# Kernel optimization log

Hardware: AMD Instinct MI355X
Metric: run time of the kernel (lower is better)

The kernel has to match this reference:

```python
import jax, jax.numpy as jnp
import numpy as np

# Module hyperparams (match init_kwargs)
NUM_EXPERTS = 64
DIM = 1024
RANK = 16
ALPHA = 1.0
SCALE = ALPHA / RANK


def setup_inputs() -> dict:
    key = jax.random.key(0)
    k1, k2, k3, k4 = jax.random.split(key, 4)
    B, K, M, D, R = 8, 8, 512, DIM, RANK
    z = jax.random.normal(k1, (B, K, M, D), dtype=jnp.float32)
    A_all = jax.random.normal(k2, (NUM_EXPERTS, D, R), dtype=jnp.float32) * 0.02
    B_all = jax.random.normal(k3, (NUM_EXPERTS, R, D), dtype=jnp.float32) * 0.02
    expert_indices = jax.random.randint(k4, (K,), 0, NUM_EXPERTS, dtype=jnp.int64) if jax.config.jax_enable_x64 else jax.random.randint(k4, (K,), 0, NUM_EXPERTS, dtype=jnp.int32)
    return {"z": z, "A_all": A_all, "B_all": B_all, "expert_indices": expert_indices}


def reference(z, A_all, B_all, expert_indices):
    # Gather per-expert LoRA factors: A [K, D, R], B [K, R, D]
    A = A_all[expert_indices]
    Bm = B_all[expert_indices]
    # Low-rank down/up projection per (batch, expert)
    down = jnp.einsum('bkmd,kdr->bkmr', z, A)   # [B, K, M, R]
    up = jnp.einsum('bkmr,krd->bkmd', down, Bm)  # [B, K, M, D]
    return up * SCALE
```

## Files before the change

kernel.cpp:

```cpp
#include <hip/hip_runtime.h>
#include <hip/hip_bf16.h>

#define DD 1024
#define RR 16
#define MM 512
#define KK 8
#define BB 8
#define SCALE_F 0.0625f

#define TT 2
#define BT 8
#define TILES 8

template <int LEN, int XOR>
__device__ __forceinline__ void fold(float (&v)[32], int lane) {
    const bool hi = (lane & XOR) != 0;
#pragma unroll
    for (int i = 0; i < LEN / 2; ++i) {
        const float keep = hi ? v[2 * i + 1] : v[2 * i];
        const float send = hi ? v[2 * i] : v[2 * i + 1];
        v[i] = keep + __shfl_xor(send, XOR, 64);
    }
}

__global__ __launch_bounds__(256, 2)
void lora_down(const float* __restrict__ z, const float* __restrict__ A_all,
               const int* __restrict__ eidx, float* __restrict__ down)
{
    __shared__ float At[RR][DD];

    const int mc = blockIdx.x;
    const int b  = blockIdx.y;
    const int k  = blockIdx.z;
    const int e  = eidx[k];

    const float* __restrict__ Ae = A_all + (size_t)e * (DD * RR);

    for (int f4 = threadIdx.x; f4 < DD * RR / 4; f4 += 256) {
        const int f = f4 << 2;
        const float4 v = *reinterpret_cast<const float4*>(Ae + f);
        const int d = f >> 4, r = f & 15;
        At[r + 0][d] = v.x;
        At[r + 1][d] = v.y;
        At[r + 2][d] = v.z;
        At[r + 3][d] = v.w;
    }
    __syncthreads();

    const int wave = threadIdx.x >> 6;
    const int lane = threadIdx.x & 63;
    const size_t rowbk = ((size_t)b * KK + k) * MM;
    const int mbase = mc * 64 + wave * TT;
    const float* __restrict__ zlane = z + (rowbk + mbase) * DD + lane * 4;

    float4 bufA[TT][4], bufB[TT][4];

    auto load_tile = [&](float4 (&buf)[TT][4], int it) {
#pragma unroll
        for (int t = 0; t < TT; ++t) {
            const float* p = zlane + (size_t)(it * BT + t) * DD;
#pragma unroll
            for (int s = 0; s < 4; ++s)
                buf[t][s] = *reinterpret_cast<const float4*>(p + s * 256);
        }
    };

    auto compute_store = [&](const float4 (&buf)[TT][4], int it) {
        float v[32];
#pragma unroll
        for (int i = 0; i < 32; ++i) v[i] = 0.f;
#pragma unroll
        for (int s = 0; s < 4; ++s) {
            const int dbase = s * 256 + lane * 4;
#pragma unroll
            for (int r = 0; r < RR; ++r) {
                const float4 a = *reinterpret_cast<const float4*>(&At[r][dbase]);
#pragma unroll
                for (int t = 0; t < TT; ++t) {
                    const float4 zv = buf[t][s];
                    float acc = v[t * 16 + r];
                    acc = fmaf(zv.x, a.x, acc);
                    acc = fmaf(zv.y, a.y, acc);
                    acc = fmaf(zv.z, a.z, acc);
                    acc = fmaf(zv.w, a.w, acc);
                    v[t * 16 + r] = acc;
                }
            }
        }
        fold<32, 1>(v, lane);
        fold<16, 2>(v, lane);
        fold<8, 4>(v, lane);
        fold<4, 8>(v, lane);
        fold<2, 16>(v, lane);
        const float total = v[0] + __shfl_xor(v[0], 32, 64);
        if (lane < 32)
            down[(rowbk + mbase + it * BT) * RR + lane] = total;
    };

    load_tile(bufA, 0);
#pragma unroll 1
    for (int ip = 0; ip < TILES / 2; ++ip) {
        load_tile(bufB, 2 * ip + 1);
        compute_store(bufA, 2 * ip);
        if (ip < TILES / 2 - 1) load_tile(bufA, 2 * ip + 2);
        compute_store(bufB, 2 * ip + 1);
    }
}

__global__ __launch_bounds__(256, 2)
void lora_up(const float* __restrict__ down, const float* __restrict__ B_all,
             const int* __restrict__ eidx, float* __restrict__ out)
{
    __shared__ float Bl[RR][DD];

    const int mc = blockIdx.x;
    const int b  = blockIdx.y;
    const int k  = blockIdx.z;
    const int e  = eidx[k];

    const float* __restrict__ Be = B_all + (size_t)e * (RR * DD);
    for (int f4 = threadIdx.x; f4 < RR * DD / 4; f4 += 256)
        *reinterpret_cast<float4*>(&Bl[0][0] + (f4 << 2)) =
            *reinterpret_cast<const float4*>(Be + (f4 << 2));
    __syncthreads();

    const int wave = threadIdx.x >> 6;
    const int lane = threadIdx.x & 63;
    const size_t rowbk = ((size_t)b * KK + k) * MM;
    const int mbase = mc * 64 + wave * TT;

    float cA[32], cB[32];

    auto load_c = [&](float (&c)[32], int it) {
        const float4* dp = reinterpret_cast<const float4*>(down + (rowbk + mbase + it * BT) * RR);
#pragma unroll
        for (int i = 0; i < 8; ++i) {
            const float4 v = dp[i];
            c[i * 4 + 0] = v.x;
            c[i * 4 + 1] = v.y;
            c[i * 4 + 2] = v.z;
            c[i * 4 + 3] = v.w;
        }
    };

    auto compute_store = [&](const float (&c)[32], int it) {
#pragma unroll
        for (int s = 0; s < 4; ++s) {
            const int dbase = s * 256 + lane * 4;
            float4 o[TT];
#pragma unroll
            for (int t = 0; t < TT; ++t) o[t] = make_float4(0.f, 0.f, 0.f, 0.f);
#pragma unroll
            for (int r = 0; r < RR; ++r) {
                const float4 bv = *reinterpret_cast<const float4*>(&Bl[r][dbase]);
#pragma unroll
                for (int t = 0; t < TT; ++t) {
                    const float cf = c[t * 16 + r];
                    o[t].x = fmaf(cf, bv.x, o[t].x);
                    o[t].y = fmaf(cf, bv.y, o[t].y);
                    o[t].z = fmaf(cf, bv.z, o[t].z);
                    o[t].w = fmaf(cf, bv.w, o[t].w);
                }
            }
#pragma unroll
            for (int t = 0; t < TT; ++t) {
                float4 res;
                res.x = o[t].x * SCALE_F;
                res.y = o[t].y * SCALE_F;
                res.z = o[t].z * SCALE_F;
                res.w = o[t].w * SCALE_F;
                *reinterpret_cast<float4*>(out + (rowbk + mbase + it * BT + t) * DD + dbase) = res;
            }
        }
    };

    load_c(cA, 0);
#pragma unroll 1
    for (int ip = 0; ip < TILES / 2; ++ip) {
        load_c(cB, 2 * ip + 1);
        compute_store(cA, 2 * ip);
        if (ip < TILES / 2 - 1) load_c(cA, 2 * ip + 2);
        compute_store(cB, 2 * ip + 1);
    }
}

extern "C" void kernel_launch(void* const* d_in, const int* in_sizes, int n_in,
                              void* d_out, int out_size, void* d_ws, size_t ws_size,
                              hipStream_t stream) {
    const float* z     = (const float*)d_in[0];
    const float* A_all = (const float*)d_in[1];
    const float* B_all = (const float*)d_in[2];
    const int*   eidx  = (const int*)d_in[3];
    float* out  = (float*)d_out;
    float* down = (float*)d_ws;

    dim3 grid(MM / 64, BB, KK);
    dim3 block(256);

    lora_down<<<grid, block, 0, stream>>>(z, A_all, eidx, down);
    lora_up<<<grid, block, 0, stream>>>(down, B_all, eidx, out);
}
```

Before: 512.0 us.

## Fuse LoRA down and up projections into one kernel with half-D shared tiles

Merges the down and up projection kernels into one. The down result stays in shared memory instead of going through a global workspace. Each block now handles 32 rows and loads the expert A and B factors in two half-width shared tiles, so shared memory use drops and more blocks can fit per CU (launch bounds raised to 4). The trade-off is that A and B are reloaded more often per row, and extra barriers are added between the phases.

```diff
diff --git a/kernel.cpp b/kernel.cpp
--- a/kernel.cpp
+++ b/kernel.cpp
@@ -2,15 +2,14 @@
 #include <hip/hip_bf16.h>
 
 #define DD 1024
+#define HD 512
 #define RR 16
 #define MM 512
 #define KK 8
 #define BB 8
+#define RB 32
 #define SCALE_F 0.0625f
-
-#define TT 2
-#define BT 8
-#define TILES 8
+#define LDP (HD + 4)
 
 template <int LEN, int XOR>
 __device__ __forceinline__ void fold(float (&v)[32], int lane) {
@@ -23,164 +22,133 @@
     }
 }
 
-__global__ __launch_bounds__(256, 2)
-void lora_down(const float* __restrict__ z, const float* __restrict__ A_all,
-               const int* __restrict__ eidx, float* __restrict__ down)
+__global__ __launch_bounds__(256, 4)
+void lora_fused(const float* __restrict__ z, const float* __restrict__ A_all,
+                const float* __restrict__ B_all, const int* __restrict__ eidx,
+                float* __restrict__ out)
 {
-    __shared__ float At[RR][DD];
+    __shared__ float Sh[RR][LDP];
+    __shared__ float dn[RB][RR];
 
-    const int mc = blockIdx.x;
-    const int b  = blockIdx.y;
-    const int k  = blockIdx.z;
-    const int e  = eidx[k];
+    const int mc = blockIdx.x, b = blockIdx.y, k = blockIdx.z;
+    const int e = eidx[k];
+    const int tid  = threadIdx.x;
+    const int wave = tid >> 6, lane = tid & 63;
+
+    const size_t rowbase = ((size_t)b * KK + k) * MM + (size_t)mc * RB;
+    const int wrow = wave * 8;
 
     const float* __restrict__ Ae = A_all + (size_t)e * (DD * RR);
+    const float* __restrict__ Be = B_all + (size_t)e * (RR * DD);
 
-    for (int f4 = threadIdx.x; f4 < DD * RR / 4; f4 += 256) {
-        const int f = f4 << 2;
-        const float4 v = *reinterpret_cast<const float4*>(Ae + f);
-        const int d = f >> 4, r = f & 15;
-        At[r + 0][d] = v.x;
-        At[r + 1][d] = v.y;
-        At[r + 2][d] = v.z;
-        At[r + 3][d] = v.w;
-    }
-    __syncthreads();
+#pragma unroll 1
+    for (int h = 0; h < 2; ++h) {
+        for (int idx = tid; idx < HD * RR / 4; idx += 256) {
+            const int f = h * (HD * RR) + idx * 4;
+            const float4 v4 = *reinterpret_cast<const float4*>(Ae + f);
+            const int d = (f >> 4) - h * HD;
+            const int r = f & 15;
+            Sh[r + 0][d] = v4.x; Sh[r + 1][d] = v4.y;
+            Sh[r + 2][d] = v4.z; Sh[r + 3][d] = v4.w;
+        }
+        __syncthreads();
 
-    const int wave = threadIdx.x >> 6;
-    const int lane = threadIdx.x & 63;
-    const size_t rowbk = ((size_t)b * KK + k) * MM;
-    const int mbase = mc * 64 + wave * TT;
-    const float* __restrict__ zlane = z + (rowbk + mbase) * DD + lane * 4;
+        const float* zl = z + (rowbase + wrow) * DD + h * HD + lane * 4;
+        float4 bufA[2][2], bufB[2][2];
 
-    float4 bufA[TT][4], bufB[TT][4];
-
-    auto load_tile = [&](float4 (&buf)[TT][4], int it) {
+        auto ldt = [&](float4 (&bf)[2][2], int t0) {
 #pragma unroll
-        for (int t = 0; t < TT; ++t) {
-            const float* p = zlane + (size_t)(it * BT + t) * DD;
+            for (int t = 0; t < 2; ++t)
 #pragma unroll
-            for (int s = 0; s < 4; ++s)
-                buf[t][s] = *reinterpret_cast<const float4*>(p + s * 256);
-        }
-    };
-
-    auto compute_store = [&](const float4 (&buf)[TT][4], int it) {
-        float v[32];
+                for (int s = 0; s < 2; ++s)
+                    bf[t][s] = *reinterpret_cast<const float4*>(
+                        zl + (size_t)(t0 + t) * DD + s * 256);
+        };
+        auto cmp = [&](const float4 (&bf)[2][2], int t0) {
+            float v[32];
 #pragma unroll
-        for (int i = 0; i < 32; ++i) v[i] = 0.f;
+            for (int i = 0; i < 32; ++i) v[i] = 0.f;
 #pragma unroll
-        for (int s = 0; s < 4; ++s) {
-            const int dbase = s * 256 + lane * 4;
+            for (int s = 0; s < 2; ++s) {
+                const int dbase = s * 256 + lane * 4;
 #pragma unroll
-            for (int r = 0; r < RR; ++r) {
-                const float4 a = *reinterpret_cast<const float4*>(&At[r][dbase]);
+                for (int r = 0; r < RR; ++r) {
+                    const float4 a = *reinterpret_cast<const float4*>(&Sh[r][dbase]);
 #pragma unroll
-                for (int t = 0; t < TT; ++t) {
-                    const float4 zv = buf[t][s];
-                    float acc = v[t * 16 + r];
-                    acc = fmaf(zv.x, a.x, acc);
-                    acc = fmaf(zv.y, a.y, acc);
-                    acc = fmaf(zv.z, a.z, acc);
-                    acc = fmaf(zv.w, a.w, acc);
-                    v[t * 16 + r] = acc;
+                    for (int t = 0; t < 2; ++t) {
+                        float acc = v[t * 16 + r];
+                        acc = fmaf(bf[t][s].x, a.x, acc);
+                        acc = fmaf(bf[t][s].y, a.y, acc);
+                        acc = fmaf(bf[t][s].z, a.z, acc);
+                        acc = fmaf(bf[t][s].w, a.w, acc);
+                        v[t * 16 + r] = acc;
+                    }
                 }
             }
+            fold<32, 1>(v, lane); fold<16, 2>(v, lane); fold<8, 4>(v, lane);
+            fold<4, 8>(v, lane);  fold<2, 16>(v, lane);
+            const float tot = v[0] + __shfl_xor(v[0], 32, 64);
+            if (lane < 32) {
+                float* p = &dn[wrow + t0 + (lane >> 4)][lane & 15];
+                if (h == 0) *p = tot; else *p += tot;
+            }
+        };
+
+        ldt(bufA, 0);
+#pragma unroll 1
+        for (int ip = 0; ip < 2; ++ip) {
+            ldt(bufB, 4 * ip + 2);
+            cmp(bufA, 4 * ip);
+            if (ip == 0) ldt(bufA, 4);
+            cmp(bufB, 4 * ip + 2);
         }
-        fold<32, 1>(v, lane);
-        fold<16, 2>(v, lane);
-        fold<8, 4>(v, lane);
-        fold<4, 8>(v, lane);
-        fold<2, 16>(v, lane);
-        const float total = v[0] + __shfl_xor(v[0], 32, 64);
-        if (lane < 32)
-            down[(rowbk + mbase + it * BT) * RR + lane] = total;
-    };
+        __syncthreads();
+    }
 
-    load_tile(bufA, 0);
 #pragma unroll 1
-    for (int ip = 0; ip < TILES / 2; ++ip) {
-        load_tile(bufB, 2 * ip + 1);
-        compute_store(bufA, 2 * ip);
-        if (ip < TILES / 2 - 1) load_tile(bufA, 2 * ip + 2);
-        compute_store(bufB, 2 * ip + 1);
-    }
-}
+    for (int h = 0; h < 2; ++h) {
+        for (int idx = tid; idx < HD * RR / 4; idx += 256) {
+            const int r = idx >> 7;
+            const int doff = (idx & 127) * 4;
+            const float4 v4 = *reinterpret_cast<const float4*>(Be + r * DD + h * HD + doff);
+            *reinterpret_cast<float4*>(&Sh[r][doff]) = v4;
+        }
+        __syncthreads();
 
-__global__ __launch_bounds__(256, 2)
-void lora_up(const float* __restrict__ down, const float* __restrict__ B_all,
-             const int* __restrict__ eidx, float* __restrict__ out)
-{
-    __shared__ float Bl[RR][DD];
+        float* ol = out + (rowbase + wrow) * DD + h * HD + lane * 4;
 
-    const int mc = blockIdx.x;
-    const int b  = blockIdx.y;
-    const int k  = blockIdx.z;
-    const int e  = eidx[k];
-
-    const float* __restrict__ Be = B_all + (size_t)e * (RR * DD);
-    for (int f4 = threadIdx.x; f4 < RR * DD / 4; f4 += 256)
-        *reinterpret_cast<float4*>(&Bl[0][0] + (f4 << 2)) =
-            *reinterpret_cast<const float4*>(Be + (f4 << 2));
-    __syncthreads();
-
-    const int wave = threadIdx.x >> 6;
-    const int lane = threadIdx.x & 63;
-    const size_t rowbk = ((size_t)b * KK + k) * MM;
-    const int mbase = mc * 64 + wave * TT;
-
-    float cA[32], cB[32];
-
-    auto load_c = [&](float (&c)[32], int it) {
-        const float4* dp = reinterpret_cast<const float4*>(down + (rowbk + mbase + it * BT) * RR);
+#pragma unroll 1
+        for (int i = 0; i < 4; ++i) {
+            const int t0 = 2 * i;
+            float c0[16], c1[16];
 #pragma unroll
-        for (int i = 0; i < 8; ++i) {
-            const float4 v = dp[i];
-            c[i * 4 + 0] = v.x;
-            c[i * 4 + 1] = v.y;
-            c[i * 4 + 2] = v.z;
-            c[i * 4 + 3] = v.w;
-        }
-    };
-
-    auto compute_store = [&](const float (&c)[32], int it) {
-#pragma unroll
-        for (int s = 0; s < 4; ++s) {
-            const int dbase = s * 256 + lane * 4;
-            float4 o[TT];
-#pragma unroll
-            for (int t = 0; t < TT; ++t) o[t] = make_float4(0.f, 0.f, 0.f, 0.f);
-#pragma unroll
-            for (int r = 0; r < RR; ++r) {
-                const float4 bv = *reinterpret_cast<const float4*>(&Bl[r][dbase]);
-#pragma unroll
-                for (int t = 0; t < TT; ++t) {
-                    const float cf = c[t * 16 + r];
-                    o[t].x = fmaf(cf, bv.x, o[t].x);
-                    o[t].y = fmaf(cf, bv.y, o[t].y);
-                    o[t].z = fmaf(cf, bv.z, o[t].z);
-                    o[t].w = fmaf(cf, bv.w, o[t].w);
-                }
+            for (int q = 0; q < 4; ++q) {
+                const float4 cv0 = *reinterpret_cast<const float4*>(&dn[wrow + t0 + 0][4 * q]);
+                const float4 cv1 = *reinterpret_cast<const float4*>(&dn[wrow + t0 + 1][4 * q]);
+                c0[4 * q + 0] = cv0.x; c0[4 * q + 1] = cv0.y; c0[4 * q + 2] = cv0.z; c0[4 * q + 3] = cv0.w;
+                c1[4 * q + 0] = cv1.x; c1[4 * q + 1] = cv1.y; c1[4 * q + 2] = cv1.z; c1[4 * q + 3] = cv1.w;
             }
 #pragma unroll
-            for (int t = 0; t < TT; ++t) {
-                float4 res;
-                res.x = o[t].x * SCALE_F;
-                res.y = o[t].y * SCALE_F;
-                res.z = o[t].z * SCALE_F;
-                res.w = o[t].w * SCALE_F;
-                *reinterpret_cast<float4*>(out + (rowbk + mbase + it * BT + t) * DD + dbase) = res;
+            for (int s = 0; s < 2; ++s) {
+                const int dbase = s * 256 + lane * 4;
+                float4 o0 = make_float4(0.f, 0.f, 0.f, 0.f);
+                float4 o1 = make_float4(0.f, 0.f, 0.f, 0.f);
+#pragma unroll
+                for (int r = 0; r < RR; ++r) {
+                    const float4 bv = *reinterpret_cast<const float4*>(&Sh[r][dbase]);
+                    o0.x = fmaf(c0[r], bv.x, o0.x); o0.y = fmaf(c0[r], bv.y, o0.y);
+                    o0.z = fmaf(c0[r], bv.z, o0.z); o0.w = fmaf(c0[r], bv.w, o0.w);
+                    o1.x = fmaf(c1[r], bv.x, o1.x); o1.y = fmaf(c1[r], bv.y, o1.y);
+                    o1.z = fmaf(c1[r], bv.z, o1.z); o1.w = fmaf(c1[r], bv.w, o1.w);
+                }
+                float4 r0, r1;
+                r0.x = o0.x * SCALE_F; r0.y = o0.y * SCALE_F; r0.z = o0.z * SCALE_F; r0.w = o0.w * SCALE_F;
+                r1.x = o1.x * SCALE_F; r1.y = o1.y * SCALE_F; r1.z = o1.z * SCALE_F; r1.w = o1.w * SCALE_F;
+                *reinterpret_cast<float4*>(ol + (size_t)(t0 + 0) * DD + s * 256) = r0;
+                *reinterpret_cast<float4*>(ol + (size_t)(t0 + 1) * DD + s * 256) = r1;
             }
         }
-    };
-
-    load_c(cA, 0);
-#pragma unroll 1
-    for (int ip = 0; ip < TILES / 2; ++ip) {
-        load_c(cB, 2 * ip + 1);
-        compute_store(cA, 2 * ip);
-        if (ip < TILES / 2 - 1) load_c(cA, 2 * ip + 2);
-        compute_store(cB, 2 * ip + 1);
+        __syncthreads();
     }
 }
 
@@ -191,12 +159,10 @@
     const float* A_all = (const float*)d_in[1];
     const float* B_all = (const float*)d_in[2];
     const int*   eidx  = (const int*)d_in[3];
-    float* out  = (float*)d_out;
-    float* down = (float*)d_ws;
+    float* out = (float*)d_out;
 
-    dim3 grid(MM / 64, BB, KK);
+    dim3 grid(MM / RB, BB, KK);
     dim3 block(256);
 
-    lora_down<<<grid, block, 0, stream>>>(z, A_all, eidx, down);
-    lora_up<<<grid, block, 0, stream>>>(down, B_all, eidx, out);
+    lora_fused<<<grid, block, 0, stream>>>(z, A_all, B_all, eidx, out);
 }
```

After: 809.0 us. 58.0% more time.
